# Performance work log

Measured on AMD Instinct MI355X. Metric: run time of the kernel, lower is better.

## Reference

```python
import jax, jax.numpy as jnp
import numpy as np
from jax import lax

B, T, H, L = 64, 512, 768, 9


def setup_inputs() -> dict:
    key = jax.random.key(0)
    ks = jax.random.split(key, 6)
    return {
        "seq_out": jax.random.normal(ks[0], (B, T, H), dtype=jnp.float32),
        "mask": jnp.ones((B, T), dtype=bool),
        "W_fc": jax.random.normal(ks[1], (H, L), dtype=jnp.float32) * 0.02,
        "b_fc": jax.random.normal(ks[2], (L,), dtype=jnp.float32) * 0.02,
        "start_transitions": jax.random.normal(ks[3], (L,), dtype=jnp.float32) * 0.1,
        "end_transitions": jax.random.normal(ks[4], (L,), dtype=jnp.float32) * 0.1,
        "transitions": jax.random.normal(ks[5], (L, L), dtype=jnp.float32) * 0.1,
    }


def reference(seq_out, mask, W_fc, b_fc, start_transitions, end_transitions, transitions):
    # linear head (dropout is identity at inference)
    emissions = jnp.einsum("bth,hl->btl", seq_out, W_fc) + b_fc  # (B,T,L)

    # --- Viterbi forward pass (torchcrf semantics) ---
    score0 = start_transitions + emissions[:, 0]  # (B,L)
    emis_rest = jnp.swapaxes(emissions[:, 1:], 0, 1)  # (T-1,B,L)
    mask_rest = jnp.swapaxes(mask[:, 1:], 0, 1)       # (T-1,B)

    def step(score, inp):
        emit_t, mask_t = inp
        # (B, prev L, next L)
        full = score[:, :, None] + transitions[None, :, :] + emit_t[:, None, :]
        next_score = jnp.max(full, axis=1)
        best_prev = jnp.argmax(full, axis=1)  # (B,L) best previous tag
        new_score = jnp.where(mask_t[:, None], next_score, score)
        return new_score, best_prev

    score, history = lax.scan(step, score0, (emis_rest, mask_rest))  # history: (T-1,B,L)

    last_tag = jnp.argmax(score + end_transitions, axis=1)  # (B,)

    # --- backtrace (mask is all-ones -> every sequence has full length T) ---
    def back(tag, hist_t):
        prev = jnp.take_along_axis(hist_t, tag[:, None], axis=1)[:, 0]
        return prev, tag  # emit tag at t+1, carry tag at t

    first_tag, tags_rest = lax.scan(back, last_tag, history, reverse=True)
    tags = jnp.concatenate([first_tag[:, None], jnp.swapaxes(tags_rest, 0, 1)], axis=1)
    return tags  # (B,T) int32 best tag sequence
```

## Files before the change

### kernel.cpp

```cpp
#include <hip/hip_runtime.h>
#include <stdint.h>

typedef unsigned long long u64;

#define T_SZ 512
#define H_SZ 768
#define L_SZ 9
#define KCHUNK 96
#define NINF (-__builtin_inff())

__device__ __forceinline__ float max3f(float a, float b, float c)
{
  return fmaxf(fmaxf(a, b), c);
}

__global__ __launch_bounds__(512) void emis_kernel(
    const float* __restrict__ seq, const float* __restrict__ W,
    const float* __restrict__ bfc, float* __restrict__ emis)
{
  const int tid  = threadIdx.x;
  const int lane = tid & 63;
  const int wid  = __builtin_amdgcn_readfirstlane(tid >> 6);

  const int row = blockIdx.x * 64 + lane;
  const float* x     = seq + (size_t)row * H_SZ + wid * KCHUNK;
  const float* wbase = W + (size_t)wid * KCHUNK * L_SZ;

  float acc[L_SZ];
#pragma unroll
  for (int j = 0; j < L_SZ; ++j) acc[j] = 0.f;

#pragma unroll 2
  for (int i = 0; i < KCHUNK / 4; ++i) {
    const float4 xv = *reinterpret_cast<const float4*>(x + 4 * i);
    const float* wp = wbase + 36 * i;
    float wf[36];
#pragma unroll
    for (int q = 0; q < 9; ++q)
      *reinterpret_cast<float4*>(&wf[4 * q]) =
          *reinterpret_cast<const float4*>(wp + 4 * q);
#pragma unroll
    for (int j = 0; j < L_SZ; ++j)
      acc[j] += xv.x * wf[j] + xv.y * wf[9 + j] + xv.z * wf[18 + j] + xv.w * wf[27 + j];
  }

  __shared__ float s_part[8 * 64 * L_SZ];
  {
    float* myp = s_part + (wid * 64 + lane) * L_SZ;
#pragma unroll
    for (int j = 0; j < L_SZ; ++j) myp[j] = acc[j];
  }
  __syncthreads();

  for (int o = tid; o < 64 * L_SZ; o += 512) {
    float s = 0.f;
#pragma unroll
    for (int sg = 0; sg < 8; ++sg) s += s_part[sg * (64 * L_SZ) + o];
    emis[(size_t)blockIdx.x * (64 * L_SZ) + o] = s + bfc[o % L_SZ];
  }
}

#define ROTI(K, v) __builtin_amdgcn_mov_dpp((v), 0x120 + (K), 0xF, 0xF, true)
#define ROTF(K, v) __int_as_float(__builtin_amdgcn_mov_dpp(__float_as_int(v), 0x120 + (K), 0xF, 0xF, true))

__device__ __forceinline__ u64 comp9(u64 a, u64 b)
{
  u64 r = 0;
#pragma unroll
  for (int x = 0; x < 9; ++x) {
    const int bx = (int)((b >> (4 * x)) & 15ull);
    const u64 ax = (a >> (bx * 4)) & 15ull;
    r |= ax << (4 * x);
  }
  return r;
}
__device__ __forceinline__ int app9(u64 f, int x) { return (int)((f >> (4 * x)) & 15ull); }

__device__ __forceinline__ u64 shfl_dn64(u64 v, int d)
{
  unsigned lo = __shfl_down((unsigned)v, d, 64);
  unsigned hi = __shfl_down((unsigned)(v >> 32), d, 64);
  return ((u64)hi << 32) | lo;
}

__global__ __launch_bounds__(256) void viterbi_kernel(
    const float* __restrict__ emis, const float* __restrict__ trans,
    const float* __restrict__ startT, const float* __restrict__ endT,
    int* __restrict__ tags)
{
  const int b   = blockIdx.x;
  const int tid = threadIdx.x;

  __shared__ __align__(16) float s_emis[T_SZ * L_SZ + 32];
  __shared__ float s_score[T_SZ * L_SZ + 8];
  __shared__ float s_T16[16 * 16];
  __shared__ unsigned char s_hist[T_SZ * L_SZ];
  __shared__ int s_last;

  {
    const float4* src = reinterpret_cast<const float4*>(emis + (size_t)b * T_SZ * L_SZ);
    float4* dst = reinterpret_cast<float4*>(s_emis);
    for (int i = tid; i < (T_SZ * L_SZ) / 4; i += 256) dst[i] = src[i];
  }
  {
    const int i = tid >> 4, j = tid & 15;
    s_T16[tid] = (i < L_SZ && j < L_SZ) ? trans[i * L_SZ + j] : NINF;
  }
  __syncthreads();

  if (tid < 16) {
    const int jj  = tid;
    const int jje = (jj < L_SZ) ? jj : (L_SZ - 1);

    float Tp[16];
    {
      int xk;
      Tp[0] = s_T16[jj * 16 + jj];
#define SETTP(K) xk = ROTI(K, jj); Tp[K] = s_T16[xk * 16 + jj];
      SETTP(1)  SETTP(2)  SETTP(3)  SETTP(4)  SETTP(5)
      SETTP(6)  SETTP(7)  SETTP(8)  SETTP(9)  SETTP(10)
      SETTP(11) SETTP(12) SETTP(13) SETTP(14) SETTP(15)
#undef SETTP
    }

    float r = (jj < L_SZ) ? (startT[jje] + s_emis[jj]) : NINF;
    s_score[jj] = r;

    float e0 = s_emis[1 * L_SZ + jje];
    float e1 = s_emis[2 * L_SZ + jje];
    const float* ep = s_emis + 3 * L_SZ + jje;
    float* sp = s_score + L_SZ + jj;

#pragma unroll 2
    for (int t = 1; t < T_SZ; ++t) {
      const float e2 = *ep; ep += L_SZ;
      float a[16];
      a[0] = r + Tp[0];
#define GATH(K) a[K] = ROTF(K, r) + Tp[K];
      GATH(1)  GATH(2)  GATH(3)  GATH(4)  GATH(5)
      GATH(6)  GATH(7)  GATH(8)  GATH(9)  GATH(10)
      GATH(11) GATH(12) GATH(13) GATH(14) GATH(15)
#undef GATH
      const float m0 = max3f(a[0], a[1], a[2]);
      const float m1 = max3f(a[3], a[4], a[5]);
      const float m2 = max3f(a[6], a[7], a[8]);
      const float m3 = max3f(a[9], a[10], a[11]);
      const float m4 = max3f(a[12], a[13], a[14]);
      const float n0 = max3f(m0, m1, m2);
      const float n1 = max3f(m3, m4, a[15]);
      r = fmaxf(n0, n1) + e0;
      *sp = r; sp += L_SZ;
      e0 = e1; e1 = e2;
    }

    const float fin = r + ((jj < L_SZ) ? endT[jje] : 0.f);
    float g[16]; int gi[16];
    g[0] = fin; gi[0] = jj;
#define GFIN(K) g[K] = ROTF(K, fin); gi[K] = ROTI(K, jj);
    GFIN(1)  GFIN(2)  GFIN(3)  GFIN(4)  GFIN(5)
    GFIN(6)  GFIN(7)  GFIN(8)  GFIN(9)  GFIN(10)
    GFIN(11) GFIN(12) GFIN(13) GFIN(14) GFIN(15)
#undef GFIN
    const float q0 = max3f(g[0], g[1], g[2]);
    const float q1 = max3f(g[3], g[4], g[5]);
    const float q2 = max3f(g[6], g[7], g[8]);
    const float q3 = max3f(g[9], g[10], g[11]);
    const float q4 = max3f(g[12], g[13], g[14]);
    const float mm = fmaxf(max3f(q0, q1, q2), max3f(q3, q4, g[15]));
    int li = 99;
#pragma unroll
    for (int k = 0; k < 16; ++k) li = min(li, (g[k] == mm) ? gi[k] : 99);
    if (jj == 0) s_last = li;
  }
  __syncthreads();

  for (int p = tid; p < (T_SZ - 1) * L_SZ; p += 256) {
    const int t = p / L_SZ + 1;
    const int j = p - (t - 1) * L_SZ;
    const float e = s_emis[t * L_SZ + j];
    const float* sp2 = s_score + (t - 1) * L_SZ;
    float ci[9];
#pragma unroll
    for (int i = 0; i < 9; ++i) ci[i] = (sp2[i] + s_T16[i * 16 + j]) + e;
    const float m = fmaxf(max3f(max3f(ci[0], ci[1], ci[2]),
                                max3f(ci[3], ci[4], ci[5]),
                                max3f(ci[6], ci[7], ci[8])), ci[8]);
    int bi = 8;
#pragma unroll
    for (int i = 8; i >= 0; --i) bi = (ci[i] == m) ? i : bi;
    s_hist[t * L_SZ + j] = (unsigned char)bi;
  }
  __syncthreads();

  if (tid < 64) {
    const u64 IDENT = 0x876543210ull;
    const int k = tid;
    const int last = s_last;

    u64 f[8];
#pragma unroll
    for (int r = 0; r < 8; ++r) {
      const int s = 8 * k + r;
      u64 v = 0;
#pragma unroll
      for (int x = 0; x < 9; ++x)
        v |= (u64)(s_hist[s * L_SZ + x] & 15) << (4 * x);
      f[r] = v;
    }
    if (k == 0) f[0] = IDENT;

    u64 C = f[7];
#pragma unroll
    for (int r = 6; r >= 0; --r) C = comp9(f[r], C);

    u64 S = C;
#pragma unroll
    for (int d = 1; d < 64; d <<= 1) {
      u64 o = shfl_dn64(S, d);
      if (k + d > 63) o = IDENT;
      S = comp9(S, o);
    }
    u64 E = shfl_dn64(S, 1);
    if (k == 63) E = IDENT;

    int val = app9(E, last);
    int* ob = tags + b * T_SZ;
    ob[8 * k + 7] = val;
#pragma unroll
    for (int r = 7; r >= 0; --r) {
      val = app9(f[r], val);
      const int s = 8 * k + r;
      if (s >= 1) ob[s - 1] = val;
    }
  }
}

extern "C" void kernel_launch(void* const* d_in, const int* in_sizes, int n_in,
                              void* d_out, int out_size, void* d_ws, size_t ws_size,
                              hipStream_t stream)
{
  const float* seq   = (const float*)d_in[0];
  const float* W     = (const float*)d_in[2];
  const float* bfc   = (const float*)d_in[3];
  const float* stT   = (const float*)d_in[4];
  const float* enT   = (const float*)d_in[5];
  const float* trans = (const float*)d_in[6];

  int*   tags = (int*)d_out;
  float* emis = (float*)d_ws;

  emis_kernel<<<(T_SZ * 64) / 64, 512, 0, stream>>>(seq, W, bfc, emis);
  viterbi_kernel<<<64, 256, 0, stream>>>(emis, trans, stT, enT, tags);
}
```

Baseline: 80.42 us.

## Overlap Viterbi history computation with forward recursion in chunks; halve emis block

```diff
diff --git a/kernel.cpp b/kernel.cpp
--- a/kernel.cpp
+++ b/kernel.cpp
@@ -6,7 +6,7 @@
 #define T_SZ 512
 #define H_SZ 768
 #define L_SZ 9
-#define KCHUNK 96
+#define KCHUNK 192
 #define NINF (-__builtin_inff())
 
 __device__ __forceinline__ float max3f(float a, float b, float c)
@@ -14,7 +14,7 @@
   return fmaxf(fmaxf(a, b), c);
 }
 
-__global__ __launch_bounds__(512) void emis_kernel(
+__global__ __launch_bounds__(256) void emis_kernel(
     const float* __restrict__ seq, const float* __restrict__ W,
     const float* __restrict__ bfc, float* __restrict__ emis)
 {
@@ -44,7 +44,7 @@
       acc[j] += xv.x * wf[j] + xv.y * wf[9 + j] + xv.z * wf[18 + j] + xv.w * wf[27 + j];
   }
 
-  __shared__ float s_part[8 * 64 * L_SZ];
+  __shared__ float s_part[4 * 64 * L_SZ];
   {
     float* myp = s_part + (wid * 64 + lane) * L_SZ;
 #pragma unroll
@@ -52,11 +52,10 @@
   }
   __syncthreads();
 
-  for (int o = tid; o < 64 * L_SZ; o += 512) {
-    float s = 0.f;
-#pragma unroll
-    for (int sg = 0; sg < 8; ++sg) s += s_part[sg * (64 * L_SZ) + o];
-    emis[(size_t)blockIdx.x * (64 * L_SZ) + o] = s + bfc[o % L_SZ];
+  for (int o = tid; o < 64 * L_SZ; o += 256) {
+    const int j = o % L_SZ;
+    const float s = s_part[o] + s_part[576 + o] + s_part[1152 + o] + s_part[1728 + o];
+    emis[(size_t)blockIdx.x * (64 * L_SZ) + o] = s + bfc[j];
   }
 }
 
@@ -108,51 +107,80 @@
   }
   __syncthreads();
 
+  int jj = 0, jje = 0;
+  float Tp[16];
+  float r = 0.f, e0 = 0.f, e1 = 0.f;
+  const float* ep = nullptr;
+  float* sp = nullptr;
+
   if (tid < 16) {
-    const int jj  = tid;
-    const int jje = (jj < L_SZ) ? jj : (L_SZ - 1);
-
-    float Tp[16];
-    {
-      int xk;
-      Tp[0] = s_T16[jj * 16 + jj];
+    jj  = tid;
+    jje = (jj < L_SZ) ? jj : (L_SZ - 1);
+
+    int xk;
+    Tp[0] = s_T16[jj * 16 + jj];
 #define SETTP(K) xk = ROTI(K, jj); Tp[K] = s_T16[xk * 16 + jj];
-      SETTP(1)  SETTP(2)  SETTP(3)  SETTP(4)  SETTP(5)
-      SETTP(6)  SETTP(7)  SETTP(8)  SETTP(9)  SETTP(10)
-      SETTP(11) SETTP(12) SETTP(13) SETTP(14) SETTP(15)
+    SETTP(1)  SETTP(2)  SETTP(3)  SETTP(4)  SETTP(5)
+    SETTP(6)  SETTP(7)  SETTP(8)  SETTP(9)  SETTP(10)
+    SETTP(11) SETTP(12) SETTP(13) SETTP(14) SETTP(15)
 #undef SETTP
-    }
-
-    float r = (jj < L_SZ) ? (startT[jje] + s_emis[jj]) : NINF;
+
+    r = (jj < L_SZ) ? (startT[jje] + s_emis[jj]) : NINF;
     s_score[jj] = r;
 
-    float e0 = s_emis[1 * L_SZ + jje];
-    float e1 = s_emis[2 * L_SZ + jje];
-    const float* ep = s_emis + 3 * L_SZ + jje;
-    float* sp = s_score + L_SZ + jj;
-
+    e0 = s_emis[1 * L_SZ + jje];
+    e1 = s_emis[2 * L_SZ + jje];
+    ep = s_emis + 3 * L_SZ + jje;
+    sp = s_score + L_SZ + jj;
+  }
+
+  for (int c = 0; c < 8; ++c) {
+    if (tid < 16) {
+      const int tend = (c == 7) ? T_SZ : (64 * c + 65);
 #pragma unroll 2
-    for (int t = 1; t < T_SZ; ++t) {
-      const float e2 = *ep; ep += L_SZ;
-      float a[16];
-      a[0] = r + Tp[0];
+      for (int t = 64 * c + 1; t < tend; ++t) {
+        const float e2 = *ep; ep += L_SZ;
+        float a[16];
+        a[0] = r + Tp[0];
 #define GATH(K) a[K] = ROTF(K, r) + Tp[K];
-      GATH(1)  GATH(2)  GATH(3)  GATH(4)  GATH(5)
-      GATH(6)  GATH(7)  GATH(8)  GATH(9)  GATH(10)
-      GATH(11) GATH(12) GATH(13) GATH(14) GATH(15)
+        GATH(1)  GATH(2)  GATH(3)  GATH(4)  GATH(5)
+        GATH(6)  GATH(7)  GATH(8)  GATH(9)  GATH(10)
+        GATH(11) GATH(12) GATH(13) GATH(14) GATH(15)
 #undef GATH
-      const float m0 = max3f(a[0], a[1], a[2]);
-      const float m1 = max3f(a[3], a[4], a[5]);
-      const float m2 = max3f(a[6], a[7], a[8]);
-      const float m3 = max3f(a[9], a[10], a[11]);
-      const float m4 = max3f(a[12], a[13], a[14]);
-      const float n0 = max3f(m0, m1, m2);
-      const float n1 = max3f(m3, m4, a[15]);
-      r = fmaxf(n0, n1) + e0;
-      *sp = r; sp += L_SZ;
-      e0 = e1; e1 = e2;
-    }
-
+        const float m0 = max3f(a[0], a[1], a[2]);
+        const float m1 = max3f(a[3], a[4], a[5]);
+        const float m2 = max3f(a[6], a[7], a[8]);
+        const float m3 = max3f(a[9], a[10], a[11]);
+        const float m4 = max3f(a[12], a[13], a[14]);
+        const float n0 = max3f(m0, m1, m2);
+        const float n1 = max3f(m3, m4, a[15]);
+        r = fmaxf(n0, n1) + e0;
+        *sp = r; sp += L_SZ;
+        e0 = e1; e1 = e2;
+      }
+    } else if (tid >= 64 && c > 0) {
+      const int tbase = 64 * (c - 1);
+      for (int q = tid - 64; q < 64 * L_SZ; q += 192) {
+        const int t = tbase + 1 + q / L_SZ;
+        const int j = q - (q / L_SZ) * L_SZ;
+        const float e = s_emis[t * L_SZ + j];
+        const float* sp2 = s_score + (t - 1) * L_SZ;
+        float ci[9];
+#pragma unroll
+        for (int i = 0; i < 9; ++i) ci[i] = (sp2[i] + s_T16[i * 16 + j]) + e;
+        const float m = fmaxf(max3f(max3f(ci[0], ci[1], ci[2]),
+                                    max3f(ci[3], ci[4], ci[5]),
+                                    max3f(ci[6], ci[7], ci[8])), ci[8]);
+        int bi = 8;
+#pragma unroll
+        for (int i = 8; i >= 0; --i) bi = (ci[i] == m) ? i : bi;
+        s_hist[t * L_SZ + j] = (unsigned char)bi;
+      }
+    }
+    __syncthreads();
+  }
+
+  if (tid < 16) {
     const float fin = r + ((jj < L_SZ) ? endT[jje] : 0.f);
     float g[16]; int gi[16];
     g[0] = fin; gi[0] = jj;
@@ -172,11 +200,10 @@
     for (int k = 0; k < 16; ++k) li = min(li, (g[k] == mm) ? gi[k] : 99);
     if (jj == 0) s_last = li;
   }
-  __syncthreads();
-
-  for (int p = tid; p < (T_SZ - 1) * L_SZ; p += 256) {
-    const int t = p / L_SZ + 1;
-    const int j = p - (t - 1) * L_SZ;
+
+  for (int q = tid; q < 63 * L_SZ; q += 256) {
+    const int t = 449 + q / L_SZ;
+    const int j = q - (q / L_SZ) * L_SZ;
     const float e = s_emis[t * L_SZ + j];
     const float* sp2 = s_score + (t - 1) * L_SZ;
     float ci[9];
@@ -199,19 +226,19 @@
 
     u64 f[8];
 #pragma unroll
-    for (int r = 0; r < 8; ++r) {
-      const int s = 8 * k + r;
+    for (int r8 = 0; r8 < 8; ++r8) {
+      const int s = 8 * k + r8;
       u64 v = 0;
 #pragma unroll
       for (int x = 0; x < 9; ++x)
         v |= (u64)(s_hist[s * L_SZ + x] & 15) << (4 * x);
-      f[r] = v;
+      f[r8] = v;
     }
     if (k == 0) f[0] = IDENT;
 
     u64 C = f[7];
 #pragma unroll
-    for (int r = 6; r >= 0; --r) C = comp9(f[r], C);
+    for (int r8 = 6; r8 >= 0; --r8) C = comp9(f[r8], C);
 
     u64 S = C;
 #pragma unroll
@@ -227,9 +254,9 @@
     int* ob = tags + b * T_SZ;
     ob[8 * k + 7] = val;
 #pragma unroll
-    for (int r = 7; r >= 0; --r) {
-      val = app9(f[r], val);
-      const int s = 8 * k + r;
+    for (int r8 = 7; r8 >= 0; --r8) {
+      val = app9(f[r8], val);
+      const int s = 8 * k + r8;
       if (s >= 1) ob[s - 1] = val;
     }
   }
@@ -249,6 +276,6 @@
   int*   tags = (int*)d_out;
   float* emis = (float*)d_ws;
 
-  emis_kernel<<<(T_SZ * 64) / 64, 512, 0, stream>>>(seq, W, bfc, emis);
+  emis_kernel<<<(T_SZ * 64) / 64, 256, 0, stream>>>(seq, W, bfc, emis);
   viterbi_kernel<<<64, 256, 0, stream>>>(emis, trans, stT, enT, tags);
 }
```

Result: slower. 91.04 us (+13.2%).
